# Performance work log

Measured on AMD Instinct MI355X. Metric: run time of the kernel, lower is better.

The kernel has to match this reference:

```python
import jax, jax.numpy as jnp
import numpy as np

N_NODES = 100000
N_EDGES = 1600000
DIM_IN = 128
DIM_OUT = 128


def setup_inputs() -> dict:
    key = jax.random.key(0)
    k1, k2, k3, k4, k5 = jax.random.split(key, 5)
    x = jax.random.normal(k1, (N_NODES, DIM_IN), dtype=jnp.float32)
    # Dense kernel (glorot-style scale)
    W = jax.random.normal(k2, (DIM_IN, DIM_OUT), dtype=jnp.float32) * (1.0 / np.sqrt(DIM_IN))
    edge_vals = jax.random.uniform(k3, (N_EDGES,), dtype=jnp.float32)
    edge_rows = jax.random.randint(k4, (N_EDGES,), 0, N_NODES, dtype=jnp.int32)
    edge_cols = jax.random.randint(k5, (N_EDGES,), 0, N_NODES, dtype=jnp.int32)
    return {"x": x, "W": W, "edge_vals": edge_vals,
            "edge_rows": edge_rows, "edge_cols": edge_cols}


def reference(x, W, edge_vals, edge_rows, edge_cols):
    # Dense projection (Dense, use_bias=False): [N, dim_in] @ [dim_in, dim_out]
    h = x @ W
    # Sparse adjacency SpMM in COO form:
    # out[r] = sum_{edges e with row r} vals[e] * h[col[e]]
    msgs = edge_vals[:, None] * h[edge_cols]            # [E, dim_out]
    out = jax.ops.segment_sum(msgs, edge_rows, num_segments=N_NODES)
    return out
```

## Files before the change

kernel.cpp:

```cpp
#include <hip/hip_runtime.h>
#include <hip/hip_bf16.h>
#include <hip/hip_fp16.h>


#define DIM 128
#define RB 128
#define NB_MAX 1024
#define CH 4096
#define REG_CAP 2560
#define P2_GRID 512
#define DEPTH 4

typedef short s16x8 __attribute__((ext_vector_type(8)));
typedef float f32x4 __attribute__((ext_vector_type(4)));
typedef unsigned short u16;
typedef unsigned long long u64;
typedef u16 u16x4 __attribute__((ext_vector_type(4)));
typedef u16 u16x8 __attribute__((ext_vector_type(8)));

static __device__ __forceinline__ u16 f2bf(float f) {
  union { float f; unsigned u; } a; a.f = f;
  return (u16)((a.u + 0x7fffu + ((a.u >> 16) & 1u)) >> 16);
}
static __device__ __forceinline__ float bf_lo(unsigned u) {
  union { unsigned u; float f; } a; a.u = u << 16; return a.f;
}
static __device__ __forceinline__ float bf_hi(unsigned u) {
  union { unsigned u; float f; } a; a.u = u & 0xffff0000u; return a.f;
}
static __device__ __forceinline__ u16 f2h(float f) {
  return __half_as_ushort(__float2half(f));
}
static __device__ __forceinline__ float h2f(u16 h) {
  return __half2float(__ushort_as_half(h));
}

__global__ __launch_bounds__(256) void repack_w_kernel(
    const float* __restrict__ W, u16* __restrict__ Wp) {
  int e = blockIdx.x * 256 + threadIdx.x;
  int k = e >> 7, n = e & 127;
  Wp[((k >> 3) * 128 + n) * 8 + (k & 7)] = f2bf(W[e]);
}

static __device__ __forceinline__ void gemm_body(
    const float* __restrict__ x, const u16* __restrict__ Wp,
    u16* __restrict__ hb, int n_nodes, int m0, u16* xl) {
  const int t = threadIdx.x;

  const float4* x4 = (const float4*)x;
#pragma unroll
  for (int it = 0; it < 16; ++it) {
    int i = it * 256 + t;
    int r = i >> 5, c = i & 31;
    float4 v = make_float4(0.f, 0.f, 0.f, 0.f);
    int node = m0 + r;
    if (node < n_nodes) v = x4[(size_t)node * 32 + c];
    u16x4 pk = {f2bf(v.x), f2bf(v.y), f2bf(v.z), f2bf(v.w)};
    *(u16x4*)&xl[r * 136 + c * 4] = pk;
  }
  __syncthreads();

  const int w = t >> 6, l = t & 63, q = l >> 4, n15 = l & 15;

  f32x4 acc[2][8];
#pragma unroll
  for (int mt = 0; mt < 2; ++mt)
#pragma unroll
    for (int nt = 0; nt < 8; ++nt) acc[mt][nt] = (f32x4){0.f, 0.f, 0.f, 0.f};

#pragma unroll
  for (int ks = 0; ks < 4; ++ks) {
    s16x8 a0 = *(const s16x8*)&xl[(w * 32 + n15) * 136 + ks * 32 + q * 8];
    s16x8 a1 = *(const s16x8*)&xl[(w * 32 + 16 + n15) * 136 + ks * 32 + q * 8];
#pragma unroll
    for (int nt = 0; nt < 8; ++nt) {
      s16x8 b = *(const s16x8*)&Wp[(size_t)(((ks * 4 + q) * 128) + nt * 16 + n15) * 8];
      acc[0][nt] = __builtin_amdgcn_mfma_f32_16x16x32_bf16(a0, b, acc[0][nt], 0, 0, 0);
      acc[1][nt] = __builtin_amdgcn_mfma_f32_16x16x32_bf16(a1, b, acc[1][nt], 0, 0, 0);
    }
  }
  __syncthreads();

#pragma unroll
  for (int mt = 0; mt < 2; ++mt)
#pragma unroll
    for (int nt = 0; nt < 8; ++nt)
#pragma unroll
      for (int r_ = 0; r_ < 4; ++r_)
        xl[(w * 32 + mt * 16 + q * 4 + r_) * 136 + nt * 16 + n15] =
            f2bf(acc[mt][nt][r_]);
  __syncthreads();

#pragma unroll
  for (int it = 0; it < 8; ++it) {
    int chunk = it * 256 + t;
    int r = chunk >> 4, c = chunk & 15;
    int node = m0 + r;
    if (node < n_nodes)
      *(u16x8*)(hb + (size_t)node * 128 + c * 8) = *(const u16x8*)&xl[r * 136 + c * 8];
  }
}

static __device__ __forceinline__ void part_body(
    const int* __restrict__ rows, const int* __restrict__ cols,
    const float* __restrict__ vals, int* __restrict__ gcur,
    u64* __restrict__ reg, int n_edges, int nb, int base,
    int* hist, int* ofs, int* gbase, int* lcur, int* wsum, u64* srec) {
  const int t = threadIdx.x;
  const int lane = t & 63;
  const int wid = t >> 6;

  for (int i = t; i < NB_MAX; i += 256) { hist[i] = 0; lcur[i] = 0; }
  __syncthreads();

  int r[16], c[16];
  float v[16];
  bool ok[16];
#pragma unroll
  for (int i = 0; i < 16; ++i) {
    int e = base + i * 256 + t;
    ok[i] = e < n_edges;
    r[i] = ok[i] ? rows[e] : 0;
    c[i] = ok[i] ? cols[e] : 0;
    v[i] = ok[i] ? vals[e] : 0.f;
    if (ok[i]) atomicAdd(&hist[r[i] >> 7], 1);
  }
  __syncthreads();

  const int b0 = t * 4;
  int h0 = hist[b0], h1 = hist[b0 + 1], h2 = hist[b0 + 2], h3 = hist[b0 + 3];
  int run = h0 + h1 + h2 + h3;

  for (int b = t; b < nb; b += 256) {
    int hc = hist[b];
    gbase[b] = (hc > 0) ? atomicAdd(&gcur[b], hc) : 0;
  }

  int vsc = run;
#pragma unroll
  for (int off = 1; off < 64; off <<= 1) {
    int u = __shfl_up(vsc, off, 64);
    if (lane >= off) vsc += u;
  }
  if (lane == 63) wsum[wid] = vsc;
  __syncthreads();
  int wbase = 0;
#pragma unroll
  for (int ww = 0; ww < 3; ++ww)
    if (ww < wid) wbase += wsum[ww];
  int ex = wbase + vsc - run;
  ofs[b0] = ex;
  ofs[b0 + 1] = ex + h0;
  ofs[b0 + 2] = ex + h0 + h1;
  ofs[b0 + 3] = ex + h0 + h1 + h2;
  __syncthreads();

#pragma unroll
  for (int i = 0; i < 16; ++i) {
    if (ok[i]) {
      int bkt = r[i] >> 7;
      int pos = ofs[bkt] + atomicAdd(&lcur[bkt], 1);
      srec[pos] = ((u64)(unsigned)r[i] << 33) | ((u64)(unsigned)c[i] << 16) |
                  (u64)f2h(v[i]);
    }
  }
  __syncthreads();

  int nvalid = n_edges - base;
  if (nvalid > CH) nvalid = CH;
  for (int i = t; i < nvalid; i += 256) {
    u64 rec = srec[i];
    int row = (int)(rec >> 33);
    int bkt = row >> 7;
    int dst = gbase[bkt] + (i - ofs[bkt]);
    if (dst < REG_CAP) reg[(size_t)bkt * REG_CAP + dst] = rec;
  }
}

__global__ __launch_bounds__(256) void gemm_part_kernel(
    const float* __restrict__ x, const u16* __restrict__ Wp, u16* __restrict__ hb,
    const int* __restrict__ rows, const int* __restrict__ cols,
    const float* __restrict__ vals, int* __restrict__ gcur, u64* __restrict__ reg,
    int n_nodes, int n_edges, int nb, int gA, int gP) {
  __shared__ union {
    u16 xl[128 * 136];
    struct {
      int hist[NB_MAX];
      int ofs[NB_MAX];
      int gbase[NB_MAX];
      int lcur[NB_MAX];
      int wsum[4];
      u64 srec[CH];
    } p;
  } sh;

  int bid = blockIdx.x;
  bool isP;
  int id;
  if (gA == 2 * gP) {
    int r = bid % 3, q = bid / 3;
    isP = (r == 2);
    id = isP ? q : q * 2 + r;
  } else {
    isP = bid < gP;
    id = isP ? bid : bid - gP;
  }

  if (!isP) {
    gemm_body(x, Wp, hb, n_nodes, id * 128, sh.xl);
  } else {
    part_body(rows, cols, vals, gcur, reg, n_edges, nb, id * CH,
              sh.p.hist, sh.p.ofs, sh.p.gbase, sh.p.lcur, sh.p.wsum, sh.p.srec);
  }
}

__global__ __launch_bounds__(256) void mfma_gemm_kernel(
    const float* __restrict__ x, const u16* __restrict__ Wp,
    u16* __restrict__ hb, int n_nodes) {
  __shared__ u16 xl[128 * 136];
  gemm_body(x, Wp, hb, n_nodes, blockIdx.x * 128, xl);
}

__global__ __launch_bounds__(1024, 6) void bucket_accum_kernel(
    const u16* __restrict__ hb, const u64* __restrict__ reg,
    const int* __restrict__ gcur, float* __restrict__ out, int n_nodes, int nb) {
  __shared__ int hist[RB];
  __shared__ int ofs[RB];
  __shared__ int lcur[RB];
  __shared__ u64 srt[REG_CAP];

  const int t = threadIdx.x;
  const int lane = t & 63;
  const int w = t >> 6;
  const int q = lane >> 4;
  const int li = lane & 15;
  const int r0 = w * 8 + q * 2;

  const uint4* h4 = (const uint4*)hb;
  float4* out4 = (float4*)out;

  for (int b = blockIdx.x; b < nb; b += gridDim.x) {
    const int row0 = b * RB;

    int n_e = gcur[b];
    if (n_e > REG_CAP) n_e = REG_CAP;

    if (t < RB) { hist[t] = 0; lcur[t] = 0; }
    __syncthreads();

    u64 rr[3];
    int rl[3];
    bool ok[3];
#pragma unroll
    for (int i = 0; i < 3; ++i) {
      int j = i * 1024 + t;
      ok[i] = j < n_e;
      rr[i] = ok[i] ? reg[(size_t)b * REG_CAP + j] : 0;
      rl[i] = (int)(rr[i] >> 33) & (RB - 1);
      if (ok[i]) atomicAdd(&hist[rl[i]], 1);
    }
    __syncthreads();

    if (t < 64) {
      int h0 = hist[2 * t], h1 = hist[2 * t + 1];
      int s = h0 + h1;
      int v = s;
#pragma unroll
      for (int off = 1; off < 64; off <<= 1) {
        int u = __shfl_up(v, off, 64);
        if (t >= off) v += u;
      }
      int ex = v - s;
      ofs[2 * t] = ex;
      ofs[2 * t + 1] = ex + h0;
    }
    __syncthreads();

#pragma unroll
    for (int i = 0; i < 3; ++i) {
      if (ok[i]) {
        int pos = ofs[rl[i]] + atomicAdd(&lcur[rl[i]], 1);
        srt[pos] = rr[i];
      }
    }
    __syncthreads();

#pragma unroll
    for (int k = 0; k < 2; ++k) {
      int rli = r0 + k;
      int gr = row0 + rli;
      if (gr < n_nodes && hist[rli] == 0) {
        out4[(size_t)gr * 32 + li * 2] = make_float4(0.f, 0.f, 0.f, 0.f);
        out4[(size_t)gr * 32 + li * 2 + 1] = make_float4(0.f, 0.f, 0.f, 0.f);
      }
    }

    int qs0 = ofs[r0];
    int qs1 = ofs[r0 + 1] + hist[r0 + 1];

    if (qs1 > qs0) {
      float a0 = 0.f, a1 = 0.f, a2 = 0.f, a3 = 0.f;
      float a4 = 0.f, a5 = 0.f, a6 = 0.f, a7 = 0.f;
      int cur = (int)(srt[qs0] >> 33) & (RB - 1);

      for (int p = qs0; p < qs1; p += DEPTH) {
        uint4 uu[DEPTH];
        unsigned mv[DEPTH];
#pragma unroll
        for (int j = 0; j < DEPTH; ++j) {
          int idx = p + j;
          idx = idx < qs1 ? idx : qs1 - 1;
          u64 rec = srt[idx];
          int col = (int)((rec >> 16) & 0x1FFFF);
          mv[j] = ((unsigned)((rec >> 33) & (RB - 1)) << 16) | (unsigned)(rec & 0xFFFF);
          uu[j] = h4[(size_t)col * 16 + li];
        }
#pragma unroll
        for (int j = 0; j < DEPTH; ++j) {
          if (p + j < qs1) {
            int lr = (int)(mv[j] >> 16);
            if (lr != cur) {
              size_t o = (size_t)(row0 + cur) * 32 + li * 2;
              out4[o] = make_float4(a0, a1, a2, a3);
              out4[o + 1] = make_float4(a4, a5, a6, a7);
              a0 = a1 = a2 = a3 = a4 = a5 = a6 = a7 = 0.f;
              cur = lr;
            }
            float vv = h2f((u16)(mv[j] & 0xFFFF));
            a0 += vv * bf_lo(uu[j].x);
            a1 += vv * bf_hi(uu[j].x);
            a2 += vv * bf_lo(uu[j].y);
            a3 += vv * bf_hi(uu[j].y);
            a4 += vv * bf_lo(uu[j].z);
            a5 += vv * bf_hi(uu[j].z);
            a6 += vv * bf_lo(uu[j].w);
            a7 += vv * bf_hi(uu[j].w);
          }
        }
      }
      size_t o = (size_t)(row0 + cur) * 32 + li * 2;
      out4[o] = make_float4(a0, a1, a2, a3);
      out4[o + 1] = make_float4(a4, a5, a6, a7);
    }

    __syncthreads();
  }
}

__global__ __launch_bounds__(256) void scatter_kernel(
    const u16* __restrict__ hb, const float* __restrict__ vals,
    const int* __restrict__ rows, const int* __restrict__ cols,
    float* __restrict__ out, int n_edges) {
  const int lane = threadIdx.x & 63;
  const int wid = (blockIdx.x * blockDim.x + threadIdx.x) >> 6;
  const int nwaves = (gridDim.x * blockDim.x) >> 6;
  const unsigned* h32 = (const unsigned*)hb;
  for (int e = wid; e < n_edges; e += nwaves) {
    int r = rows[e];
    int c = cols[e];
    float v = vals[e];
    unsigned u = h32[(size_t)c * 64 + lane];
    float* op = out + (size_t)r * DIM + 2 * lane;
    atomicAdd(op, v * bf_lo(u));
    atomicAdd(op + 1, v * bf_hi(u));
  }
}

extern "C" void kernel_launch(void* const* d_in, const int* in_sizes, int n_in,
                              void* d_out, int out_size, void* d_ws, size_t ws_size,
                              hipStream_t stream) {
  const float* x = (const float*)d_in[0];
  const float* W = (const float*)d_in[1];
  const float* edge_vals = (const float*)d_in[2];
  const int* edge_rows = (const int*)d_in[3];
  const int* edge_cols = (const int*)d_in[4];
  float* out = (float*)d_out;

  const int n_nodes = in_sizes[0] / DIM;
  const int n_edges = in_sizes[2];
  const int nb = (n_nodes + RB - 1) / RB;

  char* p = (char*)d_ws;
  u16* hb = (u16*)p;   p += (((size_t)n_nodes * DIM * 2 + 15) / 16) * 16;
  u16* Wp = (u16*)p;   p += (size_t)DIM * DIM * 2;
  int* gcur = (int*)p; p += (((size_t)nb * 4 + 15) / 16) * 16;
  u64* reg = (u64*)p;  p += (size_t)nb * REG_CAP * 8;
  const size_t need = (size_t)(p - (char*)d_ws);

  repack_w_kernel<<<64, 256, 0, stream>>>(W, Wp);

  if (ws_size < need || nb > NB_MAX) {
    mfma_gemm_kernel<<<(n_nodes + 127) / 128, 256, 0, stream>>>(x, Wp, hb, n_nodes);
    hipMemsetAsync(d_out, 0, (size_t)out_size * sizeof(float), stream);
    scatter_kernel<<<2048, 256, 0, stream>>>(hb, edge_vals, edge_rows, edge_cols,
                                             out, n_edges);
    return;
  }

  hipMemsetAsync(gcur, 0, (size_t)nb * sizeof(int), stream);

  const int gA = (n_nodes + 127) / 128;
  const int gP = (n_edges + CH - 1) / CH;
  gemm_part_kernel<<<gA + gP, 256, 0, stream>>>(x, Wp, hb, edge_rows, edge_cols,
                                                edge_vals, gcur, reg, n_nodes,
                                                n_edges, nb, gA, gP);

  int p2_grid = nb < P2_GRID ? nb : P2_GRID;
  bucket_accum_kernel<<<p2_grid, 1024, 0, stream>>>(hb, reg, gcur, out,
                                                    n_nodes, nb);
}
```

Measured before the change: 230.9 us.

## Shrink partition chunks, interleave gemm/partition blocks evenly, launch one accum block per bucket

The edge chunk size per partition block drops from 4096 to 2560, so there are more, smaller partition blocks with fewer registers per thread. The gemm and partition blocks are now interleaved by proportional placement rather than a fixed 2:1 pattern. The accumulation kernel no longer uses a grid-stride loop over buckets and instead launches one block per bucket, which removes the trailing barrier. The aim is better load balance and overlap, at the cost of more blocks and more global atomics on the bucket counters.

Result: faster. 210.7 us (-8.8%).

```diff
diff --git a/kernel.cpp b/kernel.cpp
--- a/kernel.cpp
+++ b/kernel.cpp
@@ -6,9 +6,9 @@
 #define DIM 128
 #define RB 128
 #define NB_MAX 1024
-#define CH 4096
+#define CH 2560
+#define EPT (CH / 256)
 #define REG_CAP 2560
-#define P2_GRID 512
 #define DEPTH 4
 
 typedef short s16x8 __attribute__((ext_vector_type(8)));
@@ -113,11 +113,11 @@
   for (int i = t; i < NB_MAX; i += 256) { hist[i] = 0; lcur[i] = 0; }
   __syncthreads();
 
-  int r[16], c[16];
-  float v[16];
-  bool ok[16];
-#pragma unroll
-  for (int i = 0; i < 16; ++i) {
+  int r[EPT], c[EPT];
+  float v[EPT];
+  bool ok[EPT];
+#pragma unroll
+  for (int i = 0; i < EPT; ++i) {
     int e = base + i * 256 + t;
     ok[i] = e < n_edges;
     r[i] = ok[i] ? rows[e] : 0;
@@ -156,7 +156,7 @@
   __syncthreads();
 
 #pragma unroll
-  for (int i = 0; i < 16; ++i) {
+  for (int i = 0; i < EPT; ++i) {
     if (ok[i]) {
       int bkt = r[i] >> 7;
       int pos = ofs[bkt] + atomicAdd(&lcur[bkt], 1);
@@ -194,17 +194,12 @@
     } p;
   } sh;
 
-  int bid = blockIdx.x;
-  bool isP;
-  int id;
-  if (gA == 2 * gP) {
-    int r = bid % 3, q = bid / 3;
-    isP = (r == 2);
-    id = isP ? q : q * 2 + r;
-  } else {
-    isP = bid < gP;
-    id = isP ? bid : bid - gP;
-  }
+  const int bid = blockIdx.x;
+  const long long G = gA + gP;
+  const int pc0 = (int)((long long)bid * gP / G);
+  const int pc1 = (int)((long long)(bid + 1) * gP / G);
+  const bool isP = pc1 > pc0;
+  const int id = isP ? pc0 : bid - pc0;
 
   if (!isP) {
     gemm_body(x, Wp, hb, n_nodes, id * 128, sh.xl);
@@ -223,13 +218,59 @@
 
 __global__ __launch_bounds__(1024, 6) void bucket_accum_kernel(
     const u16* __restrict__ hb, const u64* __restrict__ reg,
-    const int* __restrict__ gcur, float* __restrict__ out, int n_nodes, int nb) {
+    const int* __restrict__ gcur, float* __restrict__ out, int n_nodes) {
   __shared__ int hist[RB];
   __shared__ int ofs[RB];
   __shared__ int lcur[RB];
   __shared__ u64 srt[REG_CAP];
 
   const int t = threadIdx.x;
+  const int b = blockIdx.x;
+  const int row0 = b * RB;
+
+  int n_e = gcur[b];
+  if (n_e > REG_CAP) n_e = REG_CAP;
+
+  if (t < RB) { hist[t] = 0; lcur[t] = 0; }
+  __syncthreads();
+
+  u64 rr[3];
+  int rl[3];
+  bool ok[3];
+#pragma unroll
+  for (int i = 0; i < 3; ++i) {
+    int j = i * 1024 + t;
+    ok[i] = j < n_e;
+    rr[i] = ok[i] ? reg[(size_t)b * REG_CAP + j] : 0;
+    rl[i] = (int)(rr[i] >> 33) & (RB - 1);
+    if (ok[i]) atomicAdd(&hist[rl[i]], 1);
+  }
+  __syncthreads();
+
+  if (t < 64) {
+    int h0 = hist[2 * t], h1 = hist[2 * t + 1];
+    int s = h0 + h1;
+    int v = s;
+#pragma unroll
+    for (int off = 1; off < 64; off <<= 1) {
+      int u = __shfl_up(v, off, 64);
+      if (t >= off) v += u;
+    }
+    int ex = v - s;
+    ofs[2 * t] = ex;
+    ofs[2 * t + 1] = ex + h0;
+  }
+  __syncthreads();
+
+#pragma unroll
+  for (int i = 0; i < 3; ++i) {
+    if (ok[i]) {
+      int pos = ofs[rl[i]] + atomicAdd(&lcur[rl[i]], 1);
+      srt[pos] = rr[i];
+    }
+  }
+  __syncthreads();
+
   const int lane = t & 63;
   const int w = t >> 6;
   const int q = lane >> 4;
@@ -239,111 +280,62 @@
   const uint4* h4 = (const uint4*)hb;
   float4* out4 = (float4*)out;
 
-  for (int b = blockIdx.x; b < nb; b += gridDim.x) {
-    const int row0 = b * RB;
-
-    int n_e = gcur[b];
-    if (n_e > REG_CAP) n_e = REG_CAP;
-
-    if (t < RB) { hist[t] = 0; lcur[t] = 0; }
-    __syncthreads();
-
-    u64 rr[3];
-    int rl[3];
-    bool ok[3];
-#pragma unroll
-    for (int i = 0; i < 3; ++i) {
-      int j = i * 1024 + t;
-      ok[i] = j < n_e;
-      rr[i] = ok[i] ? reg[(size_t)b * REG_CAP + j] : 0;
-      rl[i] = (int)(rr[i] >> 33) & (RB - 1);
-      if (ok[i]) atomicAdd(&hist[rl[i]], 1);
-    }
-    __syncthreads();
-
-    if (t < 64) {
-      int h0 = hist[2 * t], h1 = hist[2 * t + 1];
-      int s = h0 + h1;
-      int v = s;
-#pragma unroll
-      for (int off = 1; off < 64; off <<= 1) {
-        int u = __shfl_up(v, off, 64);
-        if (t >= off) v += u;
+#pragma unroll
+  for (int k = 0; k < 2; ++k) {
+    int rli = r0 + k;
+    int gr = row0 + rli;
+    if (gr < n_nodes && hist[rli] == 0) {
+      out4[(size_t)gr * 32 + li * 2] = make_float4(0.f, 0.f, 0.f, 0.f);
+      out4[(size_t)gr * 32 + li * 2 + 1] = make_float4(0.f, 0.f, 0.f, 0.f);
+    }
+  }
+
+  int qs0 = ofs[r0];
+  int qs1 = ofs[r0 + 1] + hist[r0 + 1];
+
+  if (qs1 > qs0) {
+    float a0 = 0.f, a1 = 0.f, a2 = 0.f, a3 = 0.f;
+    float a4 = 0.f, a5 = 0.f, a6 = 0.f, a7 = 0.f;
+    int cur = (int)(srt[qs0] >> 33) & (RB - 1);
+
+    for (int p = qs0; p < qs1; p += DEPTH) {
+      uint4 uu[DEPTH];
+      unsigned mv[DEPTH];
+#pragma unroll
+      for (int j = 0; j < DEPTH; ++j) {
+        int idx = p + j;
+        idx = idx < qs1 ? idx : qs1 - 1;
+        u64 rec = srt[idx];
+        int col = (int)((rec >> 16) & 0x1FFFF);
+        mv[j] = ((unsigned)((rec >> 33) & (RB - 1)) << 16) | (unsigned)(rec & 0xFFFF);
+        uu[j] = h4[(size_t)col * 16 + li];
       }
-      int ex = v - s;
-      ofs[2 * t] = ex;
-      ofs[2 * t + 1] = ex + h0;
-    }
-    __syncthreads();
-
-#pragma unroll
-    for (int i = 0; i < 3; ++i) {
-      if (ok[i]) {
-        int pos = ofs[rl[i]] + atomicAdd(&lcur[rl[i]], 1);
-        srt[pos] = rr[i];
-      }
-    }
-    __syncthreads();
-
-#pragma unroll
-    for (int k = 0; k < 2; ++k) {
-      int rli = r0 + k;
-      int gr = row0 + rli;
-      if (gr < n_nodes && hist[rli] == 0) {
-        out4[(size_t)gr * 32 + li * 2] = make_float4(0.f, 0.f, 0.f, 0.f);
-        out4[(size_t)gr * 32 + li * 2 + 1] = make_float4(0.f, 0.f, 0.f, 0.f);
-      }
-    }
-
-    int qs0 = ofs[r0];
-    int qs1 = ofs[r0 + 1] + hist[r0 + 1];
-
-    if (qs1 > qs0) {
-      float a0 = 0.f, a1 = 0.f, a2 = 0.f, a3 = 0.f;
-      float a4 = 0.f, a5 = 0.f, a6 = 0.f, a7 = 0.f;
-      int cur = (int)(srt[qs0] >> 33) & (RB - 1);
-
-      for (int p = qs0; p < qs1; p += DEPTH) {
-        uint4 uu[DEPTH];
-        unsigned mv[DEPTH];
-#pragma unroll
-        for (int j = 0; j < DEPTH; ++j) {
-          int idx = p + j;
-          idx = idx < qs1 ? idx : qs1 - 1;
-          u64 rec = srt[idx];
-          int col = (int)((rec >> 16) & 0x1FFFF);
-          mv[j] = ((unsigned)((rec >> 33) & (RB - 1)) << 16) | (unsigned)(rec & 0xFFFF);
-          uu[j] = h4[(size_t)col * 16 + li];
-        }
-#pragma unroll
-        for (int j = 0; j < DEPTH; ++j) {
-          if (p + j < qs1) {
-            int lr = (int)(mv[j] >> 16);
-            if (lr != cur) {
-              size_t o = (size_t)(row0 + cur) * 32 + li * 2;
-              out4[o] = make_float4(a0, a1, a2, a3);
-              out4[o + 1] = make_float4(a4, a5, a6, a7);
-              a0 = a1 = a2 = a3 = a4 = a5 = a6 = a7 = 0.f;
-              cur = lr;
-            }
-            float vv = h2f((u16)(mv[j] & 0xFFFF));
-            a0 += vv * bf_lo(uu[j].x);
-            a1 += vv * bf_hi(uu[j].x);
-            a2 += vv * bf_lo(uu[j].y);
-            a3 += vv * bf_hi(uu[j].y);
-            a4 += vv * bf_lo(uu[j].z);
-            a5 += vv * bf_hi(uu[j].z);
-            a6 += vv * bf_lo(uu[j].w);
-            a7 += vv * bf_hi(uu[j].w);
+#pragma unroll
+      for (int j = 0; j < DEPTH; ++j) {
+        if (p + j < qs1) {
+          int lr = (int)(mv[j] >> 16);
+          if (lr != cur) {
+            size_t o = (size_t)(row0 + cur) * 32 + li * 2;
+            out4[o] = make_float4(a0, a1, a2, a3);
+            out4[o + 1] = make_float4(a4, a5, a6, a7);
+            a0 = a1 = a2 = a3 = a4 = a5 = a6 = a7 = 0.f;
+            cur = lr;
           }
+          float vv = h2f((u16)(mv[j] & 0xFFFF));
+          a0 += vv * bf_lo(uu[j].x);
+          a1 += vv * bf_hi(uu[j].x);
+          a2 += vv * bf_lo(uu[j].y);
+          a3 += vv * bf_hi(uu[j].y);
+          a4 += vv * bf_lo(uu[j].z);
+          a5 += vv * bf_hi(uu[j].z);
+          a6 += vv * bf_lo(uu[j].w);
+          a7 += vv * bf_hi(uu[j].w);
         }
       }
-      size_t o = (size_t)(row0 + cur) * 32 + li * 2;
-      out4[o] = make_float4(a0, a1, a2, a3);
-      out4[o + 1] = make_float4(a4, a5, a6, a7);
-    }
-
-    __syncthreads();
+    }
+    size_t o = (size_t)(row0 + cur) * 32 + li * 2;
+    out4[o] = make_float4(a0, a1, a2, a3);
+    out4[o + 1] = make_float4(a4, a5, a6, a7);
   }
 }
 
@@ -405,7 +397,5 @@
                                                 edge_vals, gcur, reg, n_nodes,
                                                 n_edges, nb, gA, gP);
 
-  int p2_grid = nb < P2_GRID ? nb : P2_GRID;
-  bucket_accum_kernel<<<p2_grid, 1024, 0, stream>>>(hb, reg, gcur, out,
-                                                    n_nodes, nb);
-}
+  bucket_accum_kernel<<<nb, 1024, 0, stream>>>(hb, reg, gcur, out, n_nodes);
+}
```
